# Optimization experiments

Hardware: AMD Instinct MI355X
Metric: run time of the kernel (lower is better)

## Reference

```python
import jax, jax.numpy as jnp
import numpy as np

N_NODES = 50000
N_EDGES = 600000
CHANNELS = 128
HEADS = 8


def setup_inputs() -> dict:
    key = jax.random.key(0)
    k1, k2, k3 = jax.random.split(key, 3)
    x = jax.random.normal(k1, (N_NODES, CHANNELS), dtype=jnp.float32)
    edge_index = jax.random.randint(k2, (2, N_EDGES), 0, N_NODES, dtype=jnp.int32)
    att = jax.random.normal(k3, (HEADS, 2 * (CHANNELS // HEADS)), dtype=jnp.float32)
    return {"x": x, "edge_index": edge_index, "att": att}


def reference(x, edge_index, att):
    # x: [N, C], edge_index: [2, E], att: [H, 2*D] with D = C // H
    src, dst = edge_index[0], edge_index[1]
    n = x.shape[0]
    h = att.shape[0]
    d = att.shape[1] // 2

    x_src = x[src].reshape(-1, h, d)   # [E, H, D]
    x_dst = x[dst].reshape(-1, h, d)   # [E, H, D]

    # (cat([x_src, x_dst]) * att).sum(-1) == x_src @ att[:, :D] + x_dst @ att[:, D:]
    a_src, a_dst = att[:, :d], att[:, d:]
    alpha = jnp.einsum('ehd,hd->eh', x_src, a_src) + jnp.einsum('ehd,hd->eh', x_dst, a_dst)
    alpha = jnp.where(alpha >= 0, alpha, 0.2 * alpha)  # LeakyReLU(0.2)

    # segment softmax over dst; torch scatter_reduce amax includes the zero init,
    # so the per-node max is max(segment_max, 0)
    seg_max = jax.ops.segment_max(alpha, dst, num_segments=n)  # [N, H]
    seg_max = jnp.maximum(seg_max, 0.0)
    alpha = jnp.exp(alpha - seg_max[dst])
    seg_sum = jax.ops.segment_sum(alpha, dst, num_segments=n)  # [N, H]
    alpha = alpha / jnp.maximum(seg_sum[dst], 1e-10)

    # weighted scatter-add of source features
    weighted = x_src * alpha[..., None]                        # [E, H, D]
    out = jax.ops.segment_sum(weighted, dst, num_segments=n)   # [N, H, D]
    return out.reshape(n, -1)
```

## Files before the change

### kernel.cpp

```cpp
#include <hip/hip_runtime.h>

#define N_NODES  50000
#define N_EDGES  600000
#define CHANNELS 128
#define HEADS    8
#define HEAD_DIM 16
#define CAP      64

#define NBINS    256
#define CHUNK_E  1024
#define NCHUNK   ((N_EDGES + CHUNK_E - 1) / CHUNK_E)
#define SEGCAP   2816
#define NPB      200

#define LOGIT_VB ((N_NODES * (CHANNELS / 8)) / 256)
#define WPB      4

__device__ __forceinline__ unsigned bf16rne(float f) {
    unsigned u = __float_as_uint(f);
    return (u + 0x7FFFu + ((u >> 16) & 1u)) >> 16;
}

__global__ void hist_logit_kernel(const float* __restrict__ x,
                                  const float* __restrict__ att,
                                  const int*   __restrict__ dst,
                                  int*            __restrict__ hist,
                                  float*          __restrict__ ls8,
                                  float*          __restrict__ ld8,
                                  unsigned short* __restrict__ xb) {
    int b = blockIdx.x;
    int t = threadIdx.x;
    if (b < NCHUNK) {
        __shared__ int lh[NBINS];
        lh[t] = 0;
        __syncthreads();
        int base = b * CHUNK_E;
#pragma unroll
        for (int k = 0; k < 4; ++k) {
            int e = base + t + k * 256;
            if (e < N_EDGES) {
                unsigned bin = (unsigned)(dst[e] * NBINS) / N_NODES;
                atomicAdd(&lh[bin], 1);
            }
        }
        __syncthreads();
        hist[t * NCHUNK + b] = lh[t];
    } else {
        int gid = (b - NCHUNK) * 256 + t;
        int n  = gid >> 4;
        int c8 = gid & 15;
        int h  = c8 >> 1;
        int j8 = c8 & 1;

        const float4* xp = (const float4*)x + (size_t)gid * 2;
        float4 v0 = xp[0], v1 = xp[1];

        uint4 pk;
        pk.x = bf16rne(v0.x) | (bf16rne(v0.y) << 16);
        pk.y = bf16rne(v0.z) | (bf16rne(v0.w) << 16);
        pk.z = bf16rne(v1.x) | (bf16rne(v1.y) << 16);
        pk.w = bf16rne(v1.z) | (bf16rne(v1.w) << 16);
        ((uint4*)xb)[gid] = pk;

        const float4* att4 = (const float4*)att;
        float4 as0 = att4[h * 8 + j8 * 2],     as1 = att4[h * 8 + j8 * 2 + 1];
        float4 ad0 = att4[h * 8 + 4 + j8 * 2], ad1 = att4[h * 8 + 5 + j8 * 2];
        float ts = v0.x*as0.x + v0.y*as0.y + v0.z*as0.z + v0.w*as0.w
                 + v1.x*as1.x + v1.y*as1.y + v1.z*as1.z + v1.w*as1.w;
        float td = v0.x*ad0.x + v0.y*ad0.y + v0.z*ad0.z + v0.w*ad0.w
                 + v1.x*ad1.x + v1.y*ad1.y + v1.z*ad1.z + v1.w*ad1.w;
        ts += __shfl_xor(ts, 1, 2);
        td += __shfl_xor(td, 1, 2);
        if (j8 == 0) {
            ls8[n * HEADS + h] = ts;
            ld8[n * HEADS + h] = td;
        }
    }
}

__global__ void scan_kernel(const int* __restrict__ hist,
                            int* __restrict__ offm,
                            int* __restrict__ bincnt) {
    __shared__ int lds[256];
    int bin = blockIdx.x;
    int t = threadIdx.x;
    int c0 = t, c1 = t + 256, c2 = t + 512;
    int v0 = hist[bin * NCHUNK + c0];
    int v1 = (c1 < NCHUNK) ? hist[bin * NCHUNK + c1] : 0;
    int v2 = (c2 < NCHUNK) ? hist[bin * NCHUNK + c2] : 0;
    int s = v0 + v1 + v2;
    lds[t] = s;
    __syncthreads();
    for (int off = 1; off < 256; off <<= 1) {
        int u = (t >= off) ? lds[t - off] : 0;
        __syncthreads();
        lds[t] += u;
        __syncthreads();
    }
    int base = lds[t] - s;
    offm[c0 * NBINS + bin] = base;
    if (c1 < NCHUNK) offm[c1 * NBINS + bin] = base + v0;
    if (c2 < NCHUNK) offm[c2 * NBINS + bin] = base + v0 + v1;
    if (t == 255) bincnt[bin] = lds[255];
}

__global__ void binscatter_kernel(const int* __restrict__ src,
                                  const int* __restrict__ dst,
                                  const int* __restrict__ offm,
                                  unsigned*  __restrict__ ebuf) {
    __shared__ int loff[NBINS];
    __shared__ int lcnt[NBINS];
    int b = blockIdx.x;
    int t = threadIdx.x;
    loff[t] = offm[b * NBINS + t];
    lcnt[t] = 0;
    __syncthreads();
    int base = b * CHUNK_E;
#pragma unroll
    for (int k = 0; k < 4; ++k) {
        int e = base + t + k * 256;
        if (e < N_EDGES) {
            int d = dst[e];
            int s = src[e];
            unsigned bin = (unsigned)(d * NBINS) / N_NODES;
            int r = atomicAdd(&lcnt[bin], 1) + loff[bin];
            if (r < SEGCAP)
                ebuf[(size_t)bin * SEGCAP + r] = (unsigned)s | ((unsigned)d << 16);
        }
    }
}

__global__ void bucket_kernel(const unsigned* __restrict__ ebuf,
                              const int*      __restrict__ bincnt,
                              int*            __restrict__ cursor,
                              unsigned short* __restrict__ bucket) {
    __shared__ unsigned short rows[NPB * CAP];
    __shared__ int lcnt[NPB];
    int b = blockIdx.x;
    int t = threadIdx.x;
    int n0 = (b * N_NODES + NBINS - 1) / NBINS;
    int n1 = ((b + 1) * N_NODES + NBINS - 1) / NBINS;
    int nn = n1 - n0;
    if (t < NPB) lcnt[t] = 0;
    __syncthreads();
    int cnt = min(bincnt[b], SEGCAP);
    for (int i = t; i < cnt; i += 256) {
        unsigned rec = ebuf[(size_t)b * SEGCAP + i];
        int s = (int)(rec & 0xFFFFu);
        int d = (int)(rec >> 16);
        int pos = atomicAdd(&lcnt[d - n0], 1);
        if (pos < CAP) rows[(d - n0) * CAP + pos] = (unsigned short)s;
    }
    __syncthreads();
    int nq = nn * (CAP * 2 / 16);
    uint4* gdst = (uint4*)(bucket + (size_t)n0 * CAP);
    const uint4* lsrc = (const uint4*)rows;
    for (int i = t; i < nq; i += 256) gdst[i] = lsrc[i];
    if (t < nn) cursor[n0 + t] = lcnt[t];
}

__global__ void fused_gat_kernel(const unsigned short* __restrict__ xb,
                                 const float* __restrict__ ls8,
                                 const float* __restrict__ ld8,
                                 const int*   __restrict__ cursor,
                                 const unsigned short* __restrict__ bucket,
                                 float*       __restrict__ out) {
    __shared__ float s_p[WPB * CAP * HEADS];

    int wave = threadIdx.x >> 6;
    int lane = threadIdx.x & 63;
    int n = blockIdx.x * WPB + wave;
    if (n >= N_NODES) return;
    int h = lane >> 3;
    int j = lane & 7;
    int r   = lane >> 5;
    int l32 = lane & 31;
    int h2  = l32 >> 2;

    int   cnt_raw = cursor[n];
    int   myidx   = (int)bucket[(size_t)n * CAP + lane];
    float ldst    = ld8[n * HEADS + h];
    int cnt = (cnt_raw > CAP) ? CAP : cnt_raw;

    float* sp = s_p + wave * (CAP * HEADS);

    float av[8];
    float mymax = -1e30f;
#pragma unroll
    for (int k = 0; k < 8; ++k) {
        int i = j + 8 * k;
        av[k] = -1e30f;
        if (i < cnt) {
            int   s  = __shfl(myidx, i);
            float lg = ls8[s * HEADS + h] + ldst;
            float a  = (lg >= 0.0f) ? lg : 0.2f * lg;
            av[k] = a;
            mymax = fmaxf(mymax, a);
        }
    }
#pragma unroll
    for (int o = 4; o >= 1; o >>= 1) mymax = fmaxf(mymax, __shfl_xor(mymax, o, 8));
    float m = fmaxf(mymax, 0.0f);

    float myl = 0.0f;
#pragma unroll
    for (int k = 0; k < 8; ++k) {
        int i = j + 8 * k;
        if (i < cnt) {
            float p = __expf(av[k] - m);
            sp[i * HEADS + h] = p;
            myl += p;
        }
    }
#pragma unroll
    for (int o = 4; o >= 1; o >>= 1) myl += __shfl_xor(myl, o, 8);

#define LP(k) ( ((const uint2*)(xb + (size_t)__shfl(myidx, ((2*(k)+r) < cnt) ? (2*(k)+r) : 0) * CHANNELS))[l32] )
    uint2 q[8];
#pragma unroll
    for (int k = 0; k < 8; ++k) q[k] = LP(k);

    float a0 = 0.f, a1 = 0.f, a2 = 0.f, a3 = 0.f;
    int npair = (cnt + 1) >> 1;
    int k = 0;
    for (; k + 4 <= npair; k += 4) {
#pragma unroll
        for (int u = 0; u < 4; ++u) {
            int e2 = 2 * (k + u) + r;
            float p = (e2 < cnt) ? sp[e2 * HEADS + h2] : 0.0f;
            uint2 qq = q[u];
            a0 += p * __uint_as_float(qq.x << 16);
            a1 += p * __uint_as_float(qq.x & 0xFFFF0000u);
            a2 += p * __uint_as_float(qq.y << 16);
            a3 += p * __uint_as_float(qq.y & 0xFFFF0000u);
        }
#pragma unroll
        for (int u = 0; u < 4; ++u) q[u] = q[u + 4];
#pragma unroll
        for (int u = 0; u < 4; ++u) q[u + 4] = LP(k + 8 + u);
    }
    for (; k < npair; ++k) {
        int e2 = 2 * k + r;
        float p = (e2 < cnt) ? sp[e2 * HEADS + h2] : 0.0f;
        uint2 qq = q[0];
        a0 += p * __uint_as_float(qq.x << 16);
        a1 += p * __uint_as_float(qq.x & 0xFFFF0000u);
        a2 += p * __uint_as_float(qq.y << 16);
        a3 += p * __uint_as_float(qq.y & 0xFFFF0000u);
#pragma unroll
        for (int u = 0; u < 7; ++u) q[u] = q[u + 1];
    }
#undef LP

    a0 += __shfl_xor(a0, 32);
    a1 += __shfl_xor(a1, 32);
    a2 += __shfl_xor(a2, 32);
    a3 += __shfl_xor(a3, 32);

    float denom = __shfl(myl, h2 * 8);
    float inv = 1.0f / fmaxf(denom, 1e-10f);

    if (lane < 32) {
        float4 o4 = make_float4(a0 * inv, a1 * inv, a2 * inv, a3 * inv);
        ((float4*)(out + (size_t)n * CHANNELS))[l32] = o4;
    }
}

extern "C" void kernel_launch(void* const* d_in, const int* in_sizes, int n_in,
                              void* d_out, int out_size, void* d_ws, size_t ws_size,
                              hipStream_t stream) {
    const float* x   = (const float*)d_in[0];
    const int*   ei  = (const int*)  d_in[1];
    const float* att = (const float*)d_in[2];
    const int* src = ei;
    const int* dst = ei + N_EDGES;
    float* out = (float*)d_out;

    int*            hist   = (int*)d_ws;
    int*            offm   = hist + (size_t)NBINS * NCHUNK;
    int*            bincnt = offm + (size_t)NCHUNK * NBINS;
    unsigned*       ebuf   = (unsigned*)(bincnt + NBINS);
    int*            cursor = (int*)(ebuf + (size_t)NBINS * SEGCAP);
    unsigned short* bucket = (unsigned short*)(cursor + N_NODES);
    float*          ls8    = (float*)(bucket + (size_t)N_NODES * CAP);
    float*          ld8    = ls8 + (size_t)N_NODES * HEADS;
    unsigned short* xb     = (unsigned short*)(ld8 + (size_t)N_NODES * HEADS);

    hist_logit_kernel<<<NCHUNK + LOGIT_VB, 256, 0, stream>>>(
        x, att, dst, hist, ls8, ld8, xb);
    scan_kernel<<<NBINS, 256, 0, stream>>>(hist, offm, bincnt);
    binscatter_kernel<<<NCHUNK, 256, 0, stream>>>(src, dst, offm, ebuf);
    bucket_kernel<<<NBINS, 256, 0, stream>>>(ebuf, bincnt, cursor, bucket);
    fused_gat_kernel<<<(N_NODES + WPB - 1) / WPB, 64 * WPB, 0, stream>>>(
        xb, ls8, ld8, cursor, bucket, out);
}
```

Measured before the change: 137.1 us.

## Gather four edges per wave step with 16-byte bf16 loads, prefetch before softmax

The aggregation loop now splits the wave into four 16-lane groups, each reading one source row with uint4 (16-byte) loads instead of two 32-lane groups using 8-byte loads. The first four quad-row loads are issued before the logit/softmax phase so gather latency overlaps that computation. This halves the number of loop iterations and load instructions per edge. In exchange it needs two butterfly shuffle rounds for eight accumulators, a shallower rolling prefetch window, and more registers.

```diff
diff --git a/kernel.cpp b/kernel.cpp
--- a/kernel.cpp
+++ b/kernel.cpp
@@ -173,9 +173,9 @@
     if (n >= N_NODES) return;
     int h = lane >> 3;
     int j = lane & 7;
-    int r   = lane >> 5;
-    int l32 = lane & 31;
-    int h2  = l32 >> 2;
+    int r2  = lane >> 4;
+    int l16 = lane & 15;
+    int h3  = l16 >> 1;
 
     int   cnt_raw = cursor[n];
     int   myidx   = (int)bucket[(size_t)n * CAP + lane];
@@ -183,6 +183,9 @@
     int cnt = (cnt_raw > CAP) ? CAP : cnt_raw;
 
     float* sp = s_p + wave * (CAP * HEADS);
+
+#define LQ4(k) ( ((const uint4*)(xb + (size_t)__shfl(myidx, ((4*(k)+r2) < cnt) ? (4*(k)+r2) : 0) * CHANNELS))[l16] )
+    uint4 q0 = LQ4(0), q1 = LQ4(1), q2 = LQ4(2), q3 = LQ4(3);
 
     float av[8];
     float mymax = -1e30f;
@@ -215,54 +218,50 @@
 #pragma unroll
     for (int o = 4; o >= 1; o >>= 1) myl += __shfl_xor(myl, o, 8);
 
-#define LP(k) ( ((const uint2*)(xb + (size_t)__shfl(myidx, ((2*(k)+r) < cnt) ? (2*(k)+r) : 0) * CHANNELS))[l32] )
-    uint2 q[8];
-#pragma unroll
-    for (int k = 0; k < 8; ++k) q[k] = LP(k);
-
-    float a0 = 0.f, a1 = 0.f, a2 = 0.f, a3 = 0.f;
-    int npair = (cnt + 1) >> 1;
+    float a0=0.f,a1=0.f,a2=0.f,a3=0.f,a4=0.f,a5=0.f,a6=0.f,a7=0.f;
+    int nquad = (cnt + 3) >> 2;
+
+#define ACC(QQ, KK)                                                          \
+    {                                                                        \
+        int e = 4 * (KK) + r2;                                               \
+        float p = (e < cnt) ? sp[e * HEADS + h3] : 0.0f;                     \
+        a0 += p * __uint_as_float((QQ).x << 16);                             \
+        a1 += p * __uint_as_float((QQ).x & 0xFFFF0000u);                     \
+        a2 += p * __uint_as_float((QQ).y << 16);                             \
+        a3 += p * __uint_as_float((QQ).y & 0xFFFF0000u);                     \
+        a4 += p * __uint_as_float((QQ).z << 16);                             \
+        a5 += p * __uint_as_float((QQ).z & 0xFFFF0000u);                     \
+        a6 += p * __uint_as_float((QQ).w << 16);                             \
+        a7 += p * __uint_as_float((QQ).w & 0xFFFF0000u);                     \
+    }
+
     int k = 0;
-    for (; k + 4 <= npair; k += 4) {
-#pragma unroll
-        for (int u = 0; u < 4; ++u) {
-            int e2 = 2 * (k + u) + r;
-            float p = (e2 < cnt) ? sp[e2 * HEADS + h2] : 0.0f;
-            uint2 qq = q[u];
-            a0 += p * __uint_as_float(qq.x << 16);
-            a1 += p * __uint_as_float(qq.x & 0xFFFF0000u);
-            a2 += p * __uint_as_float(qq.y << 16);
-            a3 += p * __uint_as_float(qq.y & 0xFFFF0000u);
-        }
-#pragma unroll
-        for (int u = 0; u < 4; ++u) q[u] = q[u + 4];
-#pragma unroll
-        for (int u = 0; u < 4; ++u) q[u + 4] = LP(k + 8 + u);
-    }
-    for (; k < npair; ++k) {
-        int e2 = 2 * k + r;
-        float p = (e2 < cnt) ? sp[e2 * HEADS + h2] : 0.0f;
-        uint2 qq = q[0];
-        a0 += p * __uint_as_float(qq.x << 16);
-        a1 += p * __uint_as_float(qq.x & 0xFFFF0000u);
-        a2 += p * __uint_as_float(qq.y << 16);
-        a3 += p * __uint_as_float(qq.y & 0xFFFF0000u);
-#pragma unroll
-        for (int u = 0; u < 7; ++u) q[u] = q[u + 1];
-    }
-#undef LP
-
-    a0 += __shfl_xor(a0, 32);
-    a1 += __shfl_xor(a1, 32);
-    a2 += __shfl_xor(a2, 32);
-    a3 += __shfl_xor(a3, 32);
-
-    float denom = __shfl(myl, h2 * 8);
+    for (; k + 2 <= nquad; k += 2) {
+        ACC(q0, k);
+        ACC(q1, k + 1);
+        q0 = q2; q1 = q3;
+        q2 = LQ4(k + 4); q3 = LQ4(k + 5);
+    }
+    if (k < nquad) ACC(q0, k);
+#undef ACC
+#undef LQ4
+
+    a0 += __shfl_xor(a0, 16); a0 += __shfl_xor(a0, 32);
+    a1 += __shfl_xor(a1, 16); a1 += __shfl_xor(a1, 32);
+    a2 += __shfl_xor(a2, 16); a2 += __shfl_xor(a2, 32);
+    a3 += __shfl_xor(a3, 16); a3 += __shfl_xor(a3, 32);
+    a4 += __shfl_xor(a4, 16); a4 += __shfl_xor(a4, 32);
+    a5 += __shfl_xor(a5, 16); a5 += __shfl_xor(a5, 32);
+    a6 += __shfl_xor(a6, 16); a6 += __shfl_xor(a6, 32);
+    a7 += __shfl_xor(a7, 16); a7 += __shfl_xor(a7, 32);
+
+    float denom = __shfl(myl, h3 * 8);
     float inv = 1.0f / fmaxf(denom, 1e-10f);
 
-    if (lane < 32) {
-        float4 o4 = make_float4(a0 * inv, a1 * inv, a2 * inv, a3 * inv);
-        ((float4*)(out + (size_t)n * CHANNELS))[l32] = o4;
+    if (lane < 16) {
+        float4* op = (float4*)(out + (size_t)n * CHANNELS + l16 * 8);
+        op[0] = make_float4(a0 * inv, a1 * inv, a2 * inv, a3 * inv);
+        op[1] = make_float4(a4 * inv, a5 * inv, a6 * inv, a7 * inv);
     }
 }
 
```

New measurement: 138.7 us. No clear change (+1.1%).
